# Kernel optimization log

Measured on AMD Instinct MI355X. Metric: run time of the kernel, lower is better.

Reference implementation:

```python
import jax, jax.numpy as jnp
import numpy as np

B, T, V, E, H, L = 64, 512, 50000, 256, 256, 9


def _lstm_dir(x, w_ih, w_hh, b, reverse):
    # x: [B,T,I]; w_ih: [4H,I]; w_hh: [4H,H]; b: [4H]. PyTorch gate order i,f,g,o.
    Bm, Hm = x.shape[0], w_hh.shape[1]
    gx = jnp.einsum('bti,gi->btg', x, w_ih) + b  # [B,T,4H] precomputed input proj

    def step(carry, g_t):
        h, c = carry
        gates = g_t + h @ w_hh.T
        i, f, g, o = jnp.split(gates, 4, axis=-1)
        c = jax.nn.sigmoid(f) * c + jax.nn.sigmoid(i) * jnp.tanh(g)
        h = jax.nn.sigmoid(o) * jnp.tanh(c)
        return (h, c), h

    init = (jnp.zeros((Bm, Hm), x.dtype), jnp.zeros((Bm, Hm), x.dtype))
    _, hs = jax.lax.scan(step, init, jnp.swapaxes(gx, 0, 1), reverse=reverse)
    return jnp.swapaxes(hs, 0, 1)  # [B,T,H]


def _bilstm_layer(x, w_ih, w_hh, b):
    fwd = _lstm_dir(x, w_ih[0], w_hh[0], b[0], False)
    bwd = _lstm_dir(x, w_ih[1], w_hh[1], b[1], True)
    return jnp.concatenate([fwd, bwd], axis=-1)  # [B,T,2H]


def _crf_nll(emissions, labels, mask, trans, start_trans, end_trans):
    # emissions: [B,T,L]; labels: [B,T] int; mask: [B,T] (mask[:,0] assumed 1)
    maskf = mask.astype(emissions.dtype)
    # gold path score
    em_lab = jnp.take_along_axis(emissions, labels[..., None], axis=2)[..., 0]  # [B,T]
    trans_sc = trans[labels[:, :-1], labels[:, 1:]]  # [B,T-1]
    score = start_trans[labels[:, 0]] + em_lab[:, 0] \
        + jnp.sum((trans_sc + em_lab[:, 1:]) * maskf[:, 1:], axis=1)
    last_idx = jnp.sum(mask, axis=1).astype(jnp.int32) - 1
    last_lab = jnp.take_along_axis(labels, last_idx[:, None].astype(labels.dtype), axis=1)[:, 0]
    score = score + end_trans[last_lab]
    # log-partition via forward algorithm (scan over time)
    alpha0 = start_trans[None, :] + emissions[:, 0]  # [B,L]

    def step(alpha, xs):
        em_t, m_t = xs
        new = jax.nn.logsumexp(alpha[:, :, None] + trans[None], axis=1) + em_t
        alpha = jnp.where(m_t[:, None] > 0, new, alpha)
        return alpha, None

    alpha, _ = jax.lax.scan(
        step, alpha0,
        (jnp.swapaxes(emissions[:, 1:], 0, 1), jnp.swapaxes(mask[:, 1:], 0, 1)))
    logZ = jax.nn.logsumexp(alpha + end_trans[None, :], axis=1)  # [B]
    return -(score - logZ).mean()


def setup_inputs() -> dict:
    key = jax.random.key(0)
    ks = jax.random.split(key, 16)
    s = 0.05
    inp = {
        'input_ids': jax.random.randint(ks[0], (B, T), 0, V),
        'attention_mask': jnp.ones((B, T), jnp.int32),
        'labels': jax.random.randint(ks[1], (B, T), 0, L),
        'emb': jax.random.normal(ks[2], (V, E), jnp.float32) * s,
        # layer 0: input size E; layer 1: input size 2H. [dir, 4H, in]
        'w_ih0': jax.random.normal(ks[3], (2, 4 * H, E), jnp.float32) * s,
        'w_hh0': jax.random.normal(ks[4], (2, 4 * H, H), jnp.float32) * s,
        'b0': jax.random.normal(ks[5], (2, 4 * H), jnp.float32) * s,
        'w_ih1': jax.random.normal(ks[6], (2, 4 * H, 2 * H), jnp.float32) * s,
        'w_hh1': jax.random.normal(ks[7], (2, 4 * H, H), jnp.float32) * s,
        'b1': jax.random.normal(ks[8], (2, 4 * H), jnp.float32) * s,
        'lin_w': jax.random.normal(ks[9], (L, 2 * H), jnp.float32) * s,
        'lin_b': jax.random.normal(ks[10], (L,), jnp.float32) * s,
        'trans': jax.random.normal(ks[11], (L, L), jnp.float32) * 0.1,
        'start_trans': jax.random.normal(ks[12], (L,), jnp.float32) * 0.1,
        'end_trans': jax.random.normal(ks[13], (L,), jnp.float32) * 0.1,
    }
    return inp


def reference(input_ids, attention_mask, labels, emb, w_ih0, w_hh0, b0,
              w_ih1, w_hh1, b1, lin_w, lin_b, trans, start_trans, end_trans):
    x = emb[input_ids]                       # [B,T,E]
    x = _bilstm_layer(x, w_ih0, w_hh0, b0)   # [B,T,2H]
    x = _bilstm_layer(x, w_ih1, w_hh1, b1)   # [B,T,2H]
    emissions = x @ lin_w.T + lin_b          # [B,T,L]
    loss = _crf_nll(emissions, labels, attention_mask, trans, start_trans, end_trans)
    return loss
```

## Files before the change

kernel.cpp:

```cpp
#include <hip/hip_runtime.h>
#include <stdint.h>
#include <stddef.h>

#define B_ 64
#define T_ 512
#define E_ 256
#define H_ 256
#define L_ 9
#define BT (B_*T_)
#define G4 1024
#define N2 2048

typedef short    bf16x8  __attribute__((ext_vector_type(8)));
typedef float    f32x4   __attribute__((ext_vector_type(4)));
typedef int      i32x4   __attribute__((ext_vector_type(4)));
typedef int      i32x8   __attribute__((ext_vector_type(8)));

__device__ __forceinline__ unsigned short f2bf(float x){
    unsigned u = __builtin_bit_cast(unsigned, x);
    u += 0x7fffu + ((u >> 16) & 1u);
    return (unsigned short)(u >> 16);
}
__device__ __forceinline__ float bf2f(unsigned short h){
    unsigned u = ((unsigned)h) << 16;
    return __builtin_bit_cast(float, u);
}

__device__ __forceinline__ unsigned char f32_e4m3(float x){
    unsigned b = __builtin_bit_cast(unsigned, x);
    unsigned s = b >> 31;
    float a = fabsf(x);
    if (a >= 448.f) return (unsigned char)((s<<7) | 0x7E);
    int E = (int)((b>>23)&255) - 127;
    if (E < -6) E = -6;
    int qi = (int)rintf(a * exp2f((float)(3 - E)));
    if (qi >= 16){ qi >>= 1; ++E; }
    if (qi == 0) return (unsigned char)(s<<7);
    unsigned mag = (qi >= 8) ? ((((unsigned)(E + 7)) << 3) | (unsigned)(qi - 8))
                             : (unsigned)qi;
    return (unsigned char)((s<<7) | mag);
}

__device__ __forceinline__ float sigm(float x){
    return __builtin_amdgcn_rcpf(1.f + __expf(-x));
}
__device__ __forceinline__ float tanh_(float x){
    float e = __expf(2.f*x);
    return 1.f - 2.f*__builtin_amdgcn_rcpf(e + 1.f);
}

__device__ __forceinline__ void lds_load16(void* lds, const void* g){
    __builtin_amdgcn_global_load_lds(
        (const __attribute__((address_space(1))) void*)g,
        (__attribute__((address_space(3))) void*)lds, 16, 0, 0);
}

__device__ __forceinline__ void barrier_lds(){
    asm volatile("s_waitcnt lgkmcnt(0)" ::: "memory");
    __builtin_amdgcn_s_barrier();
    __builtin_amdgcn_sched_barrier(0);
}

__device__ __forceinline__ void store_out(unsigned short* p, float v){ *p = f2bf(v); }
__device__ __forceinline__ void store_out(float* p, float v){ *p = v; }

__global__ void k_embed(const int* __restrict__ ids, const float* __restrict__ emb,
                        unsigned char* __restrict__ x0){
    int bt = blockIdx.x;
    int e  = threadIdx.x;
    int id = ids[bt];
    x0[(size_t)bt*E_ + e] = f32_e4m3(emb[(size_t)id*E_ + e]);
}

__global__ void k_pack_wih(const float* __restrict__ in, unsigned char* __restrict__ out, int K){
    int p = blockIdx.y;
    int k = blockIdx.x*256 + threadIdx.x;
    int dirc = p >> 10, pp = p & 1023;
    int wv = pp >> 7, rem = pp & 127;
    int uh = (rem >> 6) & 1, g = (rem >> 4) & 3, ulx = rem & 15;
    int orig = dirc*1024 + g*256 + wv*32 + uh*16 + ulx;
    out[(size_t)p*K + k] = f32_e4m3(in[(size_t)orig*K + k]);
}

__global__ void k_pack_bias(const float* __restrict__ b, float* __restrict__ bp){
    int p = blockIdx.x*256 + threadIdx.x;
    int dirc = p >> 10, pp = p & 1023;
    int wv = pp >> 7, rem = pp & 127;
    int uh = (rem >> 6) & 1, g = (rem >> 4) & 3, ulx = rem & 15;
    int orig = dirc*1024 + g*256 + wv*32 + uh*16 + ulx;
    bp[p] = b[orig];
}

__global__ void k_pack_wfp8(const float* __restrict__ whh, unsigned char* __restrict__ wpk){
    int idx = blockIdx.x*256 + threadIdx.x;
    int lane = idx & 63;
    int uh   = (idx >> 6) & 1;
    int g    = (idx >> 7) & 3;
    int kt   = (idx >> 9) & 1;
    int wv   = (idx >> 10) & 7;
    int dir  = (idx >> 13) & 1;
    int ulx = lane & 15, hi4 = lane >> 4;
    int row = g*256 + wv*32 + uh*16 + ulx;
    int k0 = kt*128 + hi4*32;
    const float* src = whh + ((size_t)dir*G4 + row)*H_ + k0;
    unsigned char* dst = wpk + (size_t)idx*32;
    #pragma unroll
    for (int q = 0; q < 32; ++q) dst[q] = f32_e4m3(src[q]);
}

__global__ __launch_bounds__(256) void k_gemm_fp8(const unsigned char* __restrict__ A,
                                                  const unsigned char* __restrict__ Bm,
                                                  const float* __restrict__ bias,
                                                  unsigned short* __restrict__ C,
                                                  int M, int N, int K){
    __shared__ __align__(16) unsigned char As[16384];
    __shared__ __align__(16) unsigned char Bs[16384];
    int tid = threadIdx.x, lane = tid & 63, w = tid >> 6;
    int wm = w >> 1, wn = w & 1;
    int tileM = blockIdx.y * 128, tileN = blockIdx.x * 128;
    f32x4 acc[4][4] = {};
    for (int k0 = 0; k0 < K; k0 += 128){
        #pragma unroll
        for (int p = 0; p < 4; ++p){
            int idx = (p*256 + tid)*16;
            int ks = idx >> 12, rem = idx & 4095, row = rem >> 5;
            int jsrc = (rem & 16) ^ ((row & 4) << 2);
            lds_load16((char*)As + idx, A + (size_t)(tileM + row)*K + k0 + ks*32 + jsrc);
            lds_load16((char*)Bs + idx, Bm + (size_t)(tileN + row)*K + k0 + ks*32 + jsrc);
        }
        __syncthreads();
        int ks = lane >> 4, m15 = lane & 15;
        i32x8 af[4], bfv[4];
        #pragma unroll
        for (int mf = 0; mf < 4; ++mf){
            int r = wm*64 + mf*16 + m15;
            int base = ks*4096 + r*32, sw = (r & 4) << 2;
            i32x4 lo = *(const i32x4*)((const char*)As + base + sw);
            i32x4 hi = *(const i32x4*)((const char*)As + base + (16 ^ sw));
            af[mf] = __builtin_shufflevector(lo, hi, 0,1,2,3,4,5,6,7);
        }
        #pragma unroll
        for (int nf = 0; nf < 4; ++nf){
            int r = wn*64 + nf*16 + m15;
            int base = ks*4096 + r*32, sw = (r & 4) << 2;
            i32x4 lo = *(const i32x4*)((const char*)Bs + base + sw);
            i32x4 hi = *(const i32x4*)((const char*)Bs + base + (16 ^ sw));
            bfv[nf] = __builtin_shufflevector(lo, hi, 0,1,2,3,4,5,6,7);
        }
        #pragma unroll
        for (int mf = 0; mf < 4; ++mf)
            #pragma unroll
            for (int nf = 0; nf < 4; ++nf)
                acc[mf][nf] = __builtin_amdgcn_mfma_scale_f32_16x16x128_f8f6f4(
                                  af[mf], bfv[nf], acc[mf][nf],
                                  0, 0, 0, 0x7f7f7f7f, 0, 0x7f7f7f7f);
        barrier_lds();
    }
    #pragma unroll
    for (int mf = 0; mf < 4; ++mf){
        #pragma unroll
        for (int nf = 0; nf < 4; ++nf){
            int row0 = tileM + wm*64 + mf*16 + (lane >> 4)*4;
            int col  = tileN + wn*64 + nf*16 + (lane & 15);
            float bv = bias[col];
            #pragma unroll
            for (int r = 0; r < 4; ++r)
                C[(size_t)(row0 + r)*N + col] = f2bf(acc[mf][nf][r] + bv);
        }
    }
}

template<typename OutT>
__global__ __launch_bounds__(512, 2)
void k_rec_mfma(const unsigned short* __restrict__ gx,
                const unsigned char* __restrict__ wpk,
                OutT* __restrict__ out){
    int blk = blockIdx.x;
    int dir = blk & 1, bg = blk >> 1;
    int tid = threadIdx.x, lane = tid & 63, w = tid >> 6;
    int ul = lane & 15, hi4 = lane >> 4;
    int batch = bg*4 + hi4;

    __shared__ __align__(16) unsigned char hlds[2][32][16][8];
    {
        unsigned long long* hz = (unsigned long long*)hlds;
        for (int i = tid; i < 1024; i += 512) hz[i] = 0ull;
    }

    i32x8 wf[2][4][2];
    {
        const i32x8* wb = (const i32x8*)wpk;
        #pragma unroll
        for (int kt = 0; kt < 2; ++kt)
            #pragma unroll
            for (int g = 0; g < 4; ++g)
                #pragma unroll
                for (int uh = 0; uh < 2; ++uh)
                    wf[kt][g][uh] = wb[((((size_t)(dir*8 + w)*2 + kt)*4 + g)*2 + uh)*64 + lane];
    }
    __syncthreads();

    const unsigned short* gp = gx + (size_t)(batch*T_ + (dir ? T_-1 : 0))*N2
                                  + dir*1024 + w*128 + ul;
    ptrdiff_t dstep = dir ? -(ptrdiff_t)N2 : (ptrdiff_t)N2;

    unsigned short gxr[8];
    #pragma unroll
    for (int uh = 0; uh < 2; ++uh)
        #pragma unroll
        for (int g = 0; g < 4; ++g)
            gxr[uh*4+g] = gp[uh*64 + g*16];

    float c0 = 0.f, c1 = 0.f;
    int u0 = w*32 + ul, u1 = u0 + 16;
    OutT* ob = out + (size_t)batch*T_*512 + dir*256;

    for (int s = 0; s < T_; ++s){
        int buf = s & 1;
        f32x4 acc[4][2];
        #pragma unroll
        for (int g = 0; g < 4; ++g)
            #pragma unroll
            for (int uh = 0; uh < 2; ++uh)
                acc[g][uh] = (f32x4){ bf2f(gxr[uh*4+g]), 0.f, 0.f, 0.f };

        gp += dstep;
        unsigned short gxn[8];
        #pragma unroll
        for (int uh = 0; uh < 2; ++uh)
            #pragma unroll
            for (int g = 0; g < 4; ++g)
                gxn[uh*4+g] = gp[uh*64 + g*16];

        const unsigned long long* hrow = (const unsigned long long*)&hlds[buf][0][0][0];
        #pragma unroll
        for (int kt = 0; kt < 2; ++kt){
            unsigned long long a0 = hrow[(kt*16 + hi4*4 + 0)*16 + ul];
            unsigned long long a1 = hrow[(kt*16 + hi4*4 + 1)*16 + ul];
            unsigned long long a2 = hrow[(kt*16 + hi4*4 + 2)*16 + ul];
            unsigned long long a3 = hrow[(kt*16 + hi4*4 + 3)*16 + ul];
            i32x8 af = (i32x8){ (int)a0, (int)(a0>>32), (int)a1, (int)(a1>>32),
                                (int)a2, (int)(a2>>32), (int)a3, (int)(a3>>32) };
            #pragma unroll
            for (int g = 0; g < 4; ++g)
                #pragma unroll
                for (int uh = 0; uh < 2; ++uh)
                    acc[g][uh] = __builtin_amdgcn_mfma_scale_f32_16x16x128_f8f6f4(
                                     af, wf[kt][g][uh], acc[g][uh],
                                     0, 0, 0, 0x7f7f7f7f, 0, 0x7f7f7f7f);
        }

        int tt = dir ? (T_-1-s) : s;
        float h0, h1;
        {
            float xi = acc[0][0][0], xf = acc[1][0][0], xg = acc[2][0][0], xo = acc[3][0][0];
            c0 = sigm(xf)*c0 + sigm(xi)*tanh_(xg);
            h0 = sigm(xo)*tanh_(c0);
        }
        {
            float xi = acc[0][1][0], xf = acc[1][1][0], xg = acc[2][1][0], xo = acc[3][1][0];
            c1 = sigm(xf)*c1 + sigm(xi)*tanh_(xg);
            h1 = sigm(xo)*tanh_(c1);
        }

        unsigned char hb0, hb1;
#if __has_builtin(__builtin_amdgcn_cvt_pk_fp8_f32)
        {
            int pk = __builtin_amdgcn_cvt_pk_fp8_f32(h0, h1, 0, false);
            hb0 = (unsigned char)(pk & 0xff);
            hb1 = (unsigned char)((pk >> 8) & 0xff);
        }
#else
        hb0 = f32_e4m3(h0); hb1 = f32_e4m3(h1);
#endif
        hlds[buf^1][u0>>3][hi4*4][u0&7] = hb0;
        hlds[buf^1][u1>>3][hi4*4][u1&7] = hb1;

        if constexpr (sizeof(OutT) == 1){
            ((unsigned char*)ob)[(size_t)tt*512 + u0] = hb0;
            ((unsigned char*)ob)[(size_t)tt*512 + u1] = hb1;
        } else {
            store_out(&ob[(size_t)tt*512 + u0], h0);
            store_out(&ob[(size_t)tt*512 + u1], h1);
        }

        #pragma unroll
        for (int i = 0; i < 8; ++i) gxr[i] = gxn[i];
        barrier_lds();
    }
}

__global__ __launch_bounds__(256) void k_linear(const float* __restrict__ x,
                                                const float* __restrict__ w,
                                                const float* __restrict__ bias,
                                                float* __restrict__ em){
    int wv = threadIdx.x >> 6, lane = threadIdx.x & 63;
    int bt = blockIdx.x*4 + wv;
    const float4* xp = (const float4*)(x + (size_t)bt*(2*H_) + lane*8);
    float4 xa = xp[0], xb = xp[1];
    #pragma unroll
    for (int l = 0; l < L_; ++l){
        const float4* wp = (const float4*)(w + (size_t)l*(2*H_) + lane*8);
        float4 wa = wp[0], wb = wp[1];
        float p = xa.x*wa.x + xa.y*wa.y + xa.z*wa.z + xa.w*wa.w
                + xb.x*wb.x + xb.y*wb.y + xb.z*wb.z + xb.w*wb.w;
        #pragma unroll
        for (int o = 32; o; o >>= 1) p += __shfl_xor(p, o);
        if (lane == 0) em[(size_t)bt*L_ + l] = p + bias[l];
    }
}

__global__ void k_crf(const float* __restrict__ em, const int* __restrict__ labels,
                      const int* __restrict__ mask, const float* __restrict__ trans,
                      const float* __restrict__ st, const float* __restrict__ et,
                      float* __restrict__ out){
    int b = blockIdx.x, lane = threadIdx.x;
    __shared__ float tr[L_*L_];
    for (int i = lane; i < L_*L_; i += 64) tr[i] = trans[i];
    __syncthreads();
    const float* e  = em + (size_t)b*T_*L_;
    const int* lab  = labels + b*T_;
    const int* mk   = mask + b*T_;
    float sc = 0.f; int msum = 0;
    for (int t = lane; t < T_; t += 64){
        msum += mk[t];
        if (t >= 1)
            sc += (tr[lab[t-1]*L_ + lab[t]] + e[t*L_ + lab[t]]) * (float)mk[t];
    }
    #pragma unroll
    for (int o = 32; o; o >>= 1){ sc += __shfl_xor(sc, o); msum += __shfl_xor(msum, o); }
    int lj = lane < L_ ? lane : 0;
    float alpha = (lane < L_) ? (st[lj] + e[lj]) : -3.0e38f;
    for (int t = 1; t < T_; ++t){
        float v[L_]; float m = -3.0e38f;
        #pragma unroll
        for (int i = 0; i < L_; ++i){
            float ai = __shfl(alpha, i);
            v[i] = ai + tr[i*L_ + lj];
            m = fmaxf(m, v[i]);
        }
        float ssum = 0.f;
        #pragma unroll
        for (int i = 0; i < L_; ++i) ssum += __expf(v[i] - m);
        float nw = m + __logf(ssum) + e[t*L_ + lj];
        if (lane < L_ && mk[t] > 0) alpha = nw;
    }
    float av = (lane < L_) ? alpha + et[lj] : -3.0e38f;
    float m2 = av;
    #pragma unroll
    for (int o = 32; o; o >>= 1) m2 = fmaxf(m2, __shfl_xor(m2, o));
    float s2 = (lane < L_) ? __expf(av - m2) : 0.f;
    #pragma unroll
    for (int o = 32; o; o >>= 1) s2 += __shfl_xor(s2, o);
    if (lane == 0){
        float logZ = m2 + __logf(s2);
        int last = msum - 1;
        float score = sc + st[lab[0]] + e[lab[0]] + et[lab[last]];
        atomicAdd(out, (logZ - score) * (1.f/(float)B_));
    }
}

extern "C" void kernel_launch(void* const* d_in, const int* in_sizes, int n_in,
                              void* d_out, int out_size, void* d_ws, size_t ws_size,
                              hipStream_t stream){
    (void)in_sizes; (void)n_in; (void)out_size; (void)ws_size;
    const int*   ids    = (const int*)d_in[0];
    const int*   amask  = (const int*)d_in[1];
    const int*   labels = (const int*)d_in[2];
    const float* emb    = (const float*)d_in[3];
    const float* w_ih0  = (const float*)d_in[4];
    const float* w_hh0  = (const float*)d_in[5];
    const float* b0     = (const float*)d_in[6];
    const float* w_ih1  = (const float*)d_in[7];
    const float* w_hh1  = (const float*)d_in[8];
    const float* b1     = (const float*)d_in[9];
    const float* lin_w  = (const float*)d_in[10];
    const float* lin_b  = (const float*)d_in[11];
    const float* trans  = (const float*)d_in[12];
    const float* st     = (const float*)d_in[13];
    const float* et     = (const float*)d_in[14];
    float* out = (float*)d_out;

    char* ws = (char*)d_ws;
    size_t o = 0;
    auto alloc = [&](size_t bytes)->char*{
        char* p = ws + o; o = (o + bytes + 255) & ~(size_t)255; return p;
    };
    unsigned char*  x0    = (unsigned char*)alloc((size_t)BT*E_);
    unsigned char*  wih0p = (unsigned char*)alloc((size_t)N2*E_);
    unsigned char*  wih1p = (unsigned char*)alloc((size_t)N2*512);
    unsigned char*  wpk0  = (unsigned char*)alloc(16384*32);
    unsigned char*  wpk1  = (unsigned char*)alloc(16384*32);
    float*          bp0   = (float*)alloc(N2*4);
    float*          bp1   = (float*)alloc(N2*4);
    unsigned short* gx    = (unsigned short*)alloc((size_t)BT*N2*2);
    unsigned char*  xc1   = (unsigned char*)alloc((size_t)BT*512);
    float*          xc2   = (float*)alloc((size_t)BT*512*4);
    float*          em    = (float*)alloc((size_t)BT*L_*4 + 1024);

    hipMemsetAsync(d_out, 0, sizeof(float), stream);

    k_pack_wih<<<dim3(E_/256, N2), 256, 0, stream>>>(w_ih0, wih0p, E_);
    k_pack_wih<<<dim3(512/256, N2), 256, 0, stream>>>(w_ih1, wih1p, 512);
    k_pack_bias<<<N2/256, 256, 0, stream>>>(b0, bp0);
    k_pack_bias<<<N2/256, 256, 0, stream>>>(b1, bp1);
    k_pack_wfp8<<<16384/256, 256, 0, stream>>>(w_hh0, wpk0);
    k_pack_wfp8<<<16384/256, 256, 0, stream>>>(w_hh1, wpk1);
    k_embed<<<BT, E_, 0, stream>>>(ids, emb, x0);

    k_gemm_fp8<<<dim3(N2/128, BT/128), 256, 0, stream>>>(x0, wih0p, bp0, gx, BT, N2, E_);
    k_rec_mfma<unsigned char><<<32, 512, 0, stream>>>(gx, wpk0, xc1);
    k_gemm_fp8<<<dim3(N2/128, BT/128), 256, 0, stream>>>(xc1, wih1p, bp1, gx, BT, N2, 512);
    k_rec_mfma<float><<<32, 512, 0, stream>>>(gx, wpk1, xc2);

    k_linear<<<BT/4, 256, 0, stream>>>(xc2, lin_w, lin_b, em);
    k_crf<<<B_, 64, 0, stream>>>(em, labels, amask, trans, st, et, out);
}
```

Before: 1.317 ms.

## Double-buffer fp8 GEMM LDS loads, remap tiles across XCDs, store layer-2 output as bf16

The fp8 input-projection GEMM now double-buffers its A/B LDS tiles, prefetching the next K chunk while MFMAs run on the current one. It also uses a 1D grid with a block-id remap so adjacent tiles group per XCD, which is meant to improve L2 locality. Separately, the second recurrent layer writes its hidden states as bf16 instead of fp32, halving the traffic into the linear kernel. The custom barrier with lgkmcnt wait is replaced by __syncthreads, and LDS use per GEMM block doubles.

Result: no change. 1.321 ms (+0.3%).

```diff
diff --git a/kernel.cpp b/kernel.cpp
--- a/kernel.cpp
+++ b/kernel.cpp
@@ -15,6 +15,7 @@
 typedef float    f32x4   __attribute__((ext_vector_type(4)));
 typedef int      i32x4   __attribute__((ext_vector_type(4)));
 typedef int      i32x8   __attribute__((ext_vector_type(8)));
+typedef unsigned short u16x8 __attribute__((ext_vector_type(8)));
 
 __device__ __forceinline__ unsigned short f2bf(float x){
     unsigned u = __builtin_bit_cast(unsigned, x);
@@ -55,12 +56,6 @@
         (__attribute__((address_space(3))) void*)lds, 16, 0, 0);
 }
 
-__device__ __forceinline__ void barrier_lds(){
-    asm volatile("s_waitcnt lgkmcnt(0)" ::: "memory");
-    __builtin_amdgcn_s_barrier();
-    __builtin_amdgcn_sched_barrier(0);
-}
-
 __device__ __forceinline__ void store_out(unsigned short* p, float v){ *p = f2bf(v); }
 __device__ __forceinline__ void store_out(float* p, float v){ *p = v; }
 
@@ -113,38 +108,48 @@
                                                   const float* __restrict__ bias,
                                                   unsigned short* __restrict__ C,
                                                   int M, int N, int K){
-    __shared__ __align__(16) unsigned char As[16384];
-    __shared__ __align__(16) unsigned char Bs[16384];
+    __shared__ __align__(16) unsigned char As[2][16384];
+    __shared__ __align__(16) unsigned char Bs[2][16384];
     int tid = threadIdx.x, lane = tid & 63, w = tid >> 6;
     int wm = w >> 1, wn = w & 1;
-    int tileM = blockIdx.y * 128, tileN = blockIdx.x * 128;
-    f32x4 acc[4][4] = {};
-    for (int k0 = 0; k0 < K; k0 += 128){
+    int nwg = gridDim.x, qch = nwg >> 3;
+    int nid = (blockIdx.x & 7)*qch + (blockIdx.x >> 3);
+    int tileM = (nid >> 4) * 128, tileN = (nid & 15) * 128;
+    int nC = K >> 7;
+
+    auto stage = [&](int c, int buf){
         #pragma unroll
         for (int p = 0; p < 4; ++p){
             int idx = (p*256 + tid)*16;
             int ks = idx >> 12, rem = idx & 4095, row = rem >> 5;
             int jsrc = (rem & 16) ^ ((row & 4) << 2);
-            lds_load16((char*)As + idx, A + (size_t)(tileM + row)*K + k0 + ks*32 + jsrc);
-            lds_load16((char*)Bs + idx, Bm + (size_t)(tileN + row)*K + k0 + ks*32 + jsrc);
-        }
-        __syncthreads();
+            lds_load16(&As[buf][idx], A + (size_t)(tileM + row)*K + c*128 + ks*32 + jsrc);
+            lds_load16(&Bs[buf][idx], Bm + (size_t)(tileN + row)*K + c*128 + ks*32 + jsrc);
+        }
+    };
+
+    stage(0, 0);
+    __syncthreads();
+    f32x4 acc[4][4] = {};
+    for (int c = 0; c < nC; ++c){
+        int buf = c & 1;
+        if (c + 1 < nC) stage(c + 1, buf ^ 1);
         int ks = lane >> 4, m15 = lane & 15;
         i32x8 af[4], bfv[4];
         #pragma unroll
         for (int mf = 0; mf < 4; ++mf){
             int r = wm*64 + mf*16 + m15;
             int base = ks*4096 + r*32, sw = (r & 4) << 2;
-            i32x4 lo = *(const i32x4*)((const char*)As + base + sw);
-            i32x4 hi = *(const i32x4*)((const char*)As + base + (16 ^ sw));
+            i32x4 lo = *(const i32x4*)(&As[buf][base + sw]);
+            i32x4 hi = *(const i32x4*)(&As[buf][base + (16 ^ sw)]);
             af[mf] = __builtin_shufflevector(lo, hi, 0,1,2,3,4,5,6,7);
         }
         #pragma unroll
         for (int nf = 0; nf < 4; ++nf){
             int r = wn*64 + nf*16 + m15;
             int base = ks*4096 + r*32, sw = (r & 4) << 2;
-            i32x4 lo = *(const i32x4*)((const char*)Bs + base + sw);
-            i32x4 hi = *(const i32x4*)((const char*)Bs + base + (16 ^ sw));
+            i32x4 lo = *(const i32x4*)(&Bs[buf][base + sw]);
+            i32x4 hi = *(const i32x4*)(&Bs[buf][base + (16 ^ sw)]);
             bfv[nf] = __builtin_shufflevector(lo, hi, 0,1,2,3,4,5,6,7);
         }
         #pragma unroll
@@ -154,7 +159,7 @@
                 acc[mf][nf] = __builtin_amdgcn_mfma_scale_f32_16x16x128_f8f6f4(
                                   af[mf], bfv[nf], acc[mf][nf],
                                   0, 0, 0, 0x7f7f7f7f, 0, 0x7f7f7f7f);
-        barrier_lds();
+        __syncthreads();
     }
     #pragma unroll
     for (int mf = 0; mf < 4; ++mf){
@@ -286,24 +291,26 @@
 
         #pragma unroll
         for (int i = 0; i < 8; ++i) gxr[i] = gxn[i];
-        barrier_lds();
-    }
-}
-
-__global__ __launch_bounds__(256) void k_linear(const float* __restrict__ x,
+        __syncthreads();
+    }
+}
+
+__global__ __launch_bounds__(256) void k_linear(const unsigned short* __restrict__ x,
                                                 const float* __restrict__ w,
                                                 const float* __restrict__ bias,
                                                 float* __restrict__ em){
     int wv = threadIdx.x >> 6, lane = threadIdx.x & 63;
     int bt = blockIdx.x*4 + wv;
-    const float4* xp = (const float4*)(x + (size_t)bt*(2*H_) + lane*8);
-    float4 xa = xp[0], xb = xp[1];
+    u16x8 xv = *(const u16x8*)(x + (size_t)bt*(2*H_) + lane*8);
+    float xf[8];
+    #pragma unroll
+    for (int j = 0; j < 8; ++j) xf[j] = bf2f(xv[j]);
     #pragma unroll
     for (int l = 0; l < L_; ++l){
         const float4* wp = (const float4*)(w + (size_t)l*(2*H_) + lane*8);
         float4 wa = wp[0], wb = wp[1];
-        float p = xa.x*wa.x + xa.y*wa.y + xa.z*wa.z + xa.w*wa.w
-                + xb.x*wb.x + xb.y*wb.y + xb.z*wb.z + xb.w*wb.w;
+        float p = xf[0]*wa.x + xf[1]*wa.y + xf[2]*wa.z + xf[3]*wa.w
+                + xf[4]*wb.x + xf[5]*wb.y + xf[6]*wb.z + xf[7]*wb.w;
         #pragma unroll
         for (int o = 32; o; o >>= 1) p += __shfl_xor(p, o);
         if (lane == 0) em[(size_t)bt*L_ + l] = p + bias[l];
@@ -395,7 +402,7 @@
     float*          bp1   = (float*)alloc(N2*4);
     unsigned short* gx    = (unsigned short*)alloc((size_t)BT*N2*2);
     unsigned char*  xc1   = (unsigned char*)alloc((size_t)BT*512);
-    float*          xc2   = (float*)alloc((size_t)BT*512*4);
+    unsigned short* xc2   = (unsigned short*)alloc((size_t)BT*512*2);
     float*          em    = (float*)alloc((size_t)BT*L_*4 + 1024);
 
     hipMemsetAsync(d_out, 0, sizeof(float), stream);
@@ -408,10 +415,10 @@
     k_pack_wfp8<<<16384/256, 256, 0, stream>>>(w_hh1, wpk1);
     k_embed<<<BT, E_, 0, stream>>>(ids, emb, x0);
 
-    k_gemm_fp8<<<dim3(N2/128, BT/128), 256, 0, stream>>>(x0, wih0p, bp0, gx, BT, N2, E_);
+    k_gemm_fp8<<<4096, 256, 0, stream>>>(x0, wih0p, bp0, gx, BT, N2, E_);
     k_rec_mfma<unsigned char><<<32, 512, 0, stream>>>(gx, wpk0, xc1);
-    k_gemm_fp8<<<dim3(N2/128, BT/128), 256, 0, stream>>>(xc1, wih1p, bp1, gx, BT, N2, 512);
-    k_rec_mfma<float><<<32, 512, 0, stream>>>(gx, wpk1, xc2);
+    k_gemm_fp8<<<4096, 256, 0, stream>>>(xc1, wih1p, bp1, gx, BT, N2, 512);
+    k_rec_mfma<unsigned short><<<32, 512, 0, stream>>>(gx, wpk1, xc2);
 
     k_linear<<<BT/4, 256, 0, stream>>>(xc2, lin_w, lin_b, em);
     k_crf<<<B_, 64, 0, stream>>>(em, labels, amask, trans, st, et, out);
```
